# Kernel optimization log

Measured on AMD Instinct MI355X. Metric: run time of the kernel, lower is better.

The kernel has to match this reference:

```python
import jax, jax.numpy as jnp
import numpy as np

N = 50000      # nodes
E = 800000     # edges in adj1/adj2 (avg degree 16)
ED = 400000    # edges after edge-drop
IN = 256       # input feature dim
H = 128        # hidden
H2 = 256       # 2*hidden
GATE = 64


def _xavier(key, shape):
    fan_in, fan_out = shape[0], shape[1]
    lim = np.sqrt(6.0 / (fan_in + fan_out)).astype(np.float32)
    return jax.random.uniform(key, shape, jnp.float32, -lim, lim)


def setup_inputs() -> dict:
    key = jax.random.key(0)
    ks = jax.random.split(key, 20)
    d = {}
    d["x1"] = jax.random.normal(ks[0], (N, IN), jnp.float32)
    d["x2"] = jax.random.normal(ks[1], (N, IN), jnp.float32)
    d["adj1_row"] = jax.random.randint(ks[2], (E,), 0, N, jnp.int32)
    d["adj1_col"] = jax.random.randint(ks[3], (E,), 0, N, jnp.int32)
    d["adj1_val"] = jax.random.uniform(ks[4], (E,), jnp.float32)
    d["adj2_row"] = jax.random.randint(ks[5], (E,), 0, N, jnp.int32)
    d["adj2_col"] = jax.random.randint(ks[6], (E,), 0, N, jnp.int32)
    d["adj2_val"] = jax.random.uniform(ks[7], (E,), jnp.float32)
    d["drop_row"] = jax.random.randint(ks[8], (ED,), 0, N, jnp.int32)
    d["drop_col"] = jax.random.randint(ks[9], (ED,), 0, N, jnp.int32)
    d["drop_val"] = jax.random.uniform(ks[10], (ED,), jnp.float32)
    d["deg"] = jax.random.uniform(ks[11], (N, 1), jnp.float32)
    # GCN layer 0: Linear(IN -> 2H) no bias in fc, plus GCN bias + PReLU
    d["W0"] = _xavier(ks[12], (IN, H2))
    d["b0"] = jnp.zeros((H2,), jnp.float32)
    d["a0"] = jnp.full((1,), 0.25, jnp.float32)  # PReLU param
    # GCN layer 1: Linear(2H -> H)
    d["W1"] = _xavier(ks[13], (H2, H))
    d["b1"] = jnp.zeros((H,), jnp.float32)
    d["a1"] = jnp.full((1,), 0.25, jnp.float32)
    # MLP gate
    d["G1w"] = _xavier(ks[14], (H, GATE))
    d["G1b"] = jnp.zeros((GATE,), jnp.float32)
    d["G2w"] = _xavier(ks[15], (H, GATE))
    d["G2b"] = jnp.zeros((GATE,), jnp.float32)
    d["G3w"] = _xavier(ks[16], (2 * GATE + 1, 1))
    d["G3b"] = jnp.zeros((1,), jnp.float32)
    return d


def _spmm(row, col, val, x, n):
    # sparse adj @ x : gather source features, scale by edge value, scatter-add to rows
    return jax.ops.segment_sum(val[:, None] * x[col], row, num_segments=n)


def _prelu(x, a):
    return jnp.where(x >= 0, x, a * x)


def reference(x1, x2, adj1_row, adj1_col, adj1_val, adj2_row, adj2_col, adj2_val,
              drop_row, drop_col, drop_val, deg,
              W0, b0, a0, W1, b1, a1, G1w, G1b, G2w, G2b, G3w, G3b):
    n = x1.shape[0]

    def gcn(x, row, col, val, W, b, a):
        return _prelu(_spmm(row, col, val, x @ W, n) + b, a)

    def branch(x, row, col, val):
        h = jax.nn.relu(gcn(x, row, col, val, W0, b0, a0))
        return gcn(h, row, col, val, W1, b1, a1)

    # dropout on x1/x2 is identity in eval mode
    h1 = branch(x1, adj1_row, adj1_col, adj1_val)
    h2 = branch(x2, adj1_row, adj1_col, adj1_val)
    h3 = branch(x1, adj2_row, adj2_col, adj2_val)
    h4 = branch(x1, drop_row, drop_col, drop_val)

    # MLP gate on detached h1, h3, deg
    z1 = jax.lax.stop_gradient(h1) @ G1w + G1b
    z2 = jax.lax.stop_gradient(h3) @ G2w + G2b
    w = jnp.concatenate([z1, z2, jax.lax.stop_gradient(deg)], axis=1)
    beta = jax.nn.sigmoid(w @ G3w + G3b)
    return (h1, h2, h3, h4, beta)
```

## Files before the change

kernel.cpp:

```cpp
#include <hip/hip_runtime.h>
#include <hip/hip_bf16.h>

#define H2C 256
#define HDC 128
#define GATEC 64
#define FBSH 9
#define NBF 320
#define EPB 8192
#define EPBH 2048
#define CAPB 10240

typedef unsigned short ushort_t;
typedef unsigned long long ull_t;
typedef __attribute__((ext_vector_type(8))) __bf16 bf16x8;
typedef __attribute__((ext_vector_type(4))) float f32x4;

__device__ inline float bf2f(unsigned short v) {
    union { unsigned u; float f; } t; t.u = ((unsigned)v) << 16; return t.f;
}
__device__ inline unsigned short f2bf(float v) {
    __hip_bfloat16 b = __float2bfloat16(v);
    return *reinterpret_cast<unsigned short*>(&b);
}

__device__ inline void gload_lds16(const void* g, void* l) {
    __builtin_amdgcn_global_load_lds(
        (const __attribute__((address_space(1))) unsigned int*)g,
        (__attribute__((address_space(3))) unsigned int*)l, 16, 0, 0);
}

__global__ __launch_bounds__(256)
void gemm_bf16_mfma(const ushort_t* __restrict__ A, const ushort_t* __restrict__ BT,
                    ushort_t* __restrict__ C, int M, int Nn, int K)
{
    __shared__ ushort_t Alds[128 * 64];
    __shared__ ushort_t Blds[128 * 64];
    const int tid  = threadIdx.x;
    const int w    = tid >> 6;
    const int lane = tid & 63;
    const int wr   = w >> 1;
    const int wc   = w & 1;
    const int bm   = blockIdx.y * 128;
    const int bn   = blockIdx.x * 128;

    f32x4 acc[4][4] = {};

    for (int k0 = 0; k0 < K; k0 += 64) {
        #pragma unroll
        for (int i = 0; i < 4; ++i) {
            const int lin = i * 256 + tid;
            const int r = lin >> 3, p = lin & 7;
            int rm = bm + r; if (rm >= M) rm = M - 1;
            const ushort_t* ga = A + (size_t)rm * K + k0 + ((p ^ (r & 7)) << 3);
            gload_lds16(ga, &Alds[i * 2048 + w * 512]);
        }
        #pragma unroll
        for (int i = 0; i < 4; ++i) {
            const int lin = i * 256 + tid;
            const int r = lin >> 3, p = lin & 7;
            const ushort_t* gb = BT + (size_t)(bn + r) * K + k0 + ((p ^ (r & 7)) << 3);
            gload_lds16(gb, &Blds[i * 2048 + w * 512]);
        }
        __syncthreads();
        #pragma unroll
        for (int kk = 0; kk < 2; ++kk) {
            bf16x8 af[4], bfr[4];
            #pragma unroll
            for (int m = 0; m < 4; ++m) {
                const int r = wr * 64 + m * 16 + (lane & 15);
                const int s = kk * 4 + (lane >> 4);
                af[m] = *reinterpret_cast<const bf16x8*>(&Alds[r * 64 + ((s ^ (r & 7)) << 3)]);
            }
            #pragma unroll
            for (int n = 0; n < 4; ++n) {
                const int r = wc * 64 + n * 16 + (lane & 15);
                const int s = kk * 4 + (lane >> 4);
                bfr[n] = *reinterpret_cast<const bf16x8*>(&Blds[r * 64 + ((s ^ (r & 7)) << 3)]);
            }
            #pragma unroll
            for (int m = 0; m < 4; ++m)
                #pragma unroll
                for (int n = 0; n < 4; ++n)
                    acc[m][n] = __builtin_amdgcn_mfma_f32_16x16x32_bf16(
                        af[m], bfr[n], acc[m][n], 0, 0, 0);
        }
        __syncthreads();
    }

    #pragma unroll
    for (int m = 0; m < 4; ++m) {
        const int row0 = bm + wr * 64 + m * 16 + ((lane >> 4) << 2);
        #pragma unroll
        for (int n = 0; n < 4; ++n) {
            const int col = bn + wc * 64 + n * 16 + (lane & 15);
            #pragma unroll
            for (int q = 0; q < 4; ++q) {
                const int row = row0 + q;
                if (row < M) C[(size_t)row * Nn + col] = f2bf(acc[m][n][q]);
            }
        }
    }
}

__global__ __launch_bounds__(256)
void f2bf_pair_kernel(const float* __restrict__ in1, const float* __restrict__ in2,
                      ushort_t* __restrict__ out, long long n4each)
{
    long long i = (long long)blockIdx.x * blockDim.x + threadIdx.x;
    const long long stride = (long long)gridDim.x * blockDim.x;
    for (; i < 2 * n4each; i += stride) {
        const float* src = (i < n4each) ? in1 : in2;
        const long long k = (i < n4each) ? i : i - n4each;
        const float4 v = reinterpret_cast<const float4*>(src)[k];
        ushort4 o;
        o.x = f2bf(v.x); o.y = f2bf(v.y); o.z = f2bf(v.z); o.w = f2bf(v.w);
        reinterpret_cast<ushort4*>(out)[i] = o;
    }
}

__global__ __launch_bounds__(256)
void transpose_f2bf_kernel(const float* __restrict__ W, ushort_t* __restrict__ WT, int R, int Ccols)
{
    const int i = blockIdx.x * blockDim.x + threadIdx.x;
    if (i >= R * Ccols) return;
    const int c = i / R, r = i % R;
    WT[(size_t)c * R + r] = f2bf(W[(size_t)r * Ccols + c]);
}

__global__ __launch_bounds__(256)
void bucket_hist_kernel(const int* __restrict__ r0, const int* __restrict__ r1_,
                        const int* __restrict__ rD, int E, int ED, int N,
                        int* __restrict__ bcnt)
{
    __shared__ int h[NBF];
    const int tid = threadIdx.x;
    for (int t = tid; t < NBF; t += 256) h[t] = 0;
    __syncthreads();
    const long long tot = 2LL * E + ED;
    const long long base = (long long)blockIdx.x * EPBH;
    #pragma unroll
    for (int k = 0; k < EPBH / 256; ++k) {
        const long long i = base + k * 256 + tid;
        if (i < tot) {
            int vr;
            if (i < E)            vr = r0[i];
            else if (i < 2LL * E) vr = N + r1_[i - E];
            else                  vr = 2 * N + rD[i - 2LL * E];
            atomicAdd(&h[vr >> FBSH], 1);
        }
    }
    __syncthreads();
    for (int t = tid; t < NBF; t += 256)
        if (h[t]) atomicAdd(&bcnt[t], h[t]);
}

__global__ void scan_buckets_kernel(const int* __restrict__ bcnt, int nbu, int tot,
                                    int* __restrict__ boff, int* __restrict__ gcur,
                                    int* __restrict__ g, int NR)
{
    if (threadIdx.x == 0) {
        int acc = 0;
        for (int t = 0; t < nbu; ++t) { boff[t] = acc; gcur[t] = acc; acc += bcnt[t]; }
        boff[nbu] = acc;
        g[NR] = tot;
    }
}

__global__ __launch_bounds__(256)
void bucket_stage_kernel(const int* __restrict__ r0, const int* __restrict__ c0, const float* __restrict__ v0,
                         const int* __restrict__ r1, const int* __restrict__ c1, const float* __restrict__ v1,
                         const int* __restrict__ rD, const int* __restrict__ cD, const float* __restrict__ vD,
                         int E, int ED, int N,
                         int* __restrict__ gcur, ull_t* __restrict__ stg)
{
    __shared__ int hcnt[NBF];
    __shared__ int hbase[NBF];
    const int tid = threadIdx.x;
    for (int t = tid; t < NBF; t += 256) hcnt[t] = 0;
    __syncthreads();
    const long long tot = 2LL * E + ED;
    const long long base = (long long)blockIdx.x * EPB;
    #pragma unroll
    for (int k = 0; k < EPB / 256; ++k) {
        const long long i = base + k * 256 + tid;
        if (i < tot) {
            int vr;
            if (i < E)            vr = r0[i];
            else if (i < 2LL * E) vr = N + r1[i - E];
            else                  vr = 2 * N + rD[i - 2LL * E];
            atomicAdd(&hcnt[vr >> FBSH], 1);
        }
    }
    __syncthreads();
    for (int t = tid; t < NBF; t += 256) {
        const int c = hcnt[t];
        hbase[t] = c ? atomicAdd(&gcur[t], c) : 0;
        hcnt[t] = 0;
    }
    __syncthreads();
    #pragma unroll
    for (int k = 0; k < EPB / 256; ++k) {
        const long long i = base + k * 256 + tid;
        if (i < tot) {
            int vr, cc; float vv;
            if (i < E)            { vr = r0[i];                 cc = c0[i];            vv = v0[i]; }
            else if (i < 2LL * E) { vr = N + r1[i - E];         cc = c1[i - E];        vv = v1[i - E]; }
            else                  { vr = 2 * N + rD[i - 2LL * E]; cc = cD[i - 2LL * E]; vv = vD[i - 2LL * E]; }
            const int fb = vr >> FBSH;
            const int p = hbase[fb] + atomicAdd(&hcnt[fb], 1);
            stg[p] = ((ull_t)(unsigned)vr << 32) | ((unsigned)cc << 16) | f2bf(vv);
        }
    }
}

__global__ __launch_bounds__(256)
void sort_bucket_kernel(const int* __restrict__ boff, int NR,
                        const ull_t* __restrict__ stg,
                        int* __restrict__ g, unsigned* __restrict__ ecv)
{
    __shared__ int hcnt[512];
    __shared__ int hscan[512];
    __shared__ unsigned pay[CAPB];
    const int b = blockIdx.x;
    const int r0 = b << FBSH;
    if (r0 >= NR) return;
    int r1 = r0 + (1 << FBSH); if (r1 > NR) r1 = NR;
    const int nrows = r1 - r0;
    const int base = boff[b], end = boff[b + 1];
    const int bsz = end - base;
    const int tid = threadIdx.x;
    hcnt[tid] = 0; hcnt[tid + 256] = 0;
    __syncthreads();
    for (int i = base + tid; i < end; i += 256)
        atomicAdd(&hcnt[(int)(stg[i] >> 32) - r0], 1);
    __syncthreads();
    hscan[tid] = hcnt[tid]; hscan[tid + 256] = hcnt[tid + 256];
    __syncthreads();
    for (int o = 1; o < 512; o <<= 1) {
        const int a0 = (tid >= o) ? hscan[tid - o] : 0;
        const int a1 = (tid + 256 >= o) ? hscan[tid + 256 - o] : 0;
        __syncthreads();
        hscan[tid] += a0; hscan[tid + 256] += a1;
        __syncthreads();
    }
    if (tid < nrows)       g[r0 + tid]       = base + hscan[tid] - hcnt[tid];
    if (tid + 256 < nrows) g[r0 + tid + 256] = base + hscan[tid + 256] - hcnt[tid + 256];
    hcnt[tid]       = hscan[tid] - hcnt[tid];
    hcnt[tid + 256] = hscan[tid + 256] - hcnt[tid + 256];
    __syncthreads();
    if (bsz <= CAPB) {
        for (int i = base + tid; i < end; i += 256) {
            const ull_t t = stg[i];
            const int p = atomicAdd(&hcnt[(int)(t >> 32) - r0], 1);
            pay[p] = (unsigned)t;
        }
        __syncthreads();
        for (int i = tid; i < bsz; i += 256)
            ecv[base + i] = pay[i];
    } else {
        for (int i = base + tid; i < end; i += 256) {
            const ull_t t = stg[i];
            const int p = atomicAdd(&hcnt[(int)(t >> 32) - r0], 1);
            ecv[base + p] = (unsigned)t;
        }
    }
}

__global__ __launch_bounds__(256)
void spmm_f256(const int* __restrict__ rp, const unsigned* __restrict__ ecv,
               const ushort_t* __restrict__ X, ushort_t* __restrict__ Y,
               const float* __restrict__ bias, const float* __restrict__ ap, int n)
{
    const int r = blockIdx.x * 4 + (threadIdx.x >> 6);
    if (r >= n) return;
    const int lane = threadIdx.x & 63;
    const int half = lane >> 5;
    const int l    = lane & 31;
    const int s = rp[r], e = rp[r + 1];
    float acc[8] = {};
    #pragma unroll 2
    for (int j = s + half; j < e; j += 2) {
        const unsigned ev = ecv[j];
        const float v = bf2f((ushort_t)ev);
        const uint4 x = *reinterpret_cast<const uint4*>(X + (size_t)(ev >> 16) * H2C + l * 8);
        acc[0] += v * bf2f((ushort_t)x.x); acc[1] += v * bf2f((ushort_t)(x.x >> 16));
        acc[2] += v * bf2f((ushort_t)x.y); acc[3] += v * bf2f((ushort_t)(x.y >> 16));
        acc[4] += v * bf2f((ushort_t)x.z); acc[5] += v * bf2f((ushort_t)(x.z >> 16));
        acc[6] += v * bf2f((ushort_t)x.w); acc[7] += v * bf2f((ushort_t)(x.w >> 16));
    }
    #pragma unroll
    for (int k = 0; k < 8; ++k) acc[k] += __shfl_xor(acc[k], 32);
    if (half == 0) {
        const float a = ap[0];
        const int f0 = l * 8;
        const float4 b0v = *reinterpret_cast<const float4*>(bias + f0);
        const float4 b1v = *reinterpret_cast<const float4*>(bias + f0 + 4);
        const float bb[8] = {b0v.x, b0v.y, b0v.z, b0v.w, b1v.x, b1v.y, b1v.z, b1v.w};
        unsigned o[4];
        #pragma unroll
        for (int k = 0; k < 8; k += 2) {
            float tx = acc[k] + bb[k];
            float ty = acc[k + 1] + bb[k + 1];
            tx = tx >= 0.f ? tx : a * tx;  ty = ty >= 0.f ? ty : a * ty;
            tx = fmaxf(tx, 0.f);           ty = fmaxf(ty, 0.f);
            o[k >> 1] = ((unsigned)f2bf(ty) << 16) | f2bf(tx);
        }
        *reinterpret_cast<uint4*>(Y + (size_t)r * H2C + f0) = make_uint4(o[0], o[1], o[2], o[3]);
    }
}

__global__ __launch_bounds__(256)
void spmm_f128(const int* __restrict__ rp, const unsigned* __restrict__ ecv,
               const ushort_t* __restrict__ X, float* __restrict__ Y,
               const float* __restrict__ bias, const float* __restrict__ ap, int n)
{
    const int r = blockIdx.x * 4 + (threadIdx.x >> 6);
    if (r >= n) return;
    const int lane = threadIdx.x & 63;
    const int q = lane >> 4;
    const int l = lane & 15;
    const int s = rp[r], e = rp[r + 1];
    float acc[8] = {};
    #pragma unroll 2
    for (int j = s + q; j < e; j += 4) {
        const unsigned ev = ecv[j];
        const float v = bf2f((ushort_t)ev);
        const uint4 x = *reinterpret_cast<const uint4*>(X + (size_t)(ev >> 16) * HDC + l * 8);
        acc[0] += v * bf2f((ushort_t)x.x); acc[1] += v * bf2f((ushort_t)(x.x >> 16));
        acc[2] += v * bf2f((ushort_t)x.y); acc[3] += v * bf2f((ushort_t)(x.y >> 16));
        acc[4] += v * bf2f((ushort_t)x.z); acc[5] += v * bf2f((ushort_t)(x.z >> 16));
        acc[6] += v * bf2f((ushort_t)x.w); acc[7] += v * bf2f((ushort_t)(x.w >> 16));
    }
    #pragma unroll
    for (int k = 0; k < 8; ++k) {
        acc[k] += __shfl_xor(acc[k], 16);
        acc[k] += __shfl_xor(acc[k], 32);
    }
    if (q == 0) {
        const float a = ap[0];
        const int f0 = l * 8;
        const float4 b0v = *reinterpret_cast<const float4*>(bias + f0);
        const float4 b1v = *reinterpret_cast<const float4*>(bias + f0 + 4);
        const float bb[8] = {b0v.x, b0v.y, b0v.z, b0v.w, b1v.x, b1v.y, b1v.z, b1v.w};
        float o[8];
        #pragma unroll
        for (int k = 0; k < 8; ++k) {
            float t = acc[k] + bb[k];
            o[k] = t >= 0.f ? t : a * t;
        }
        *reinterpret_cast<float4*>(Y + (size_t)r * HDC + f0)     = make_float4(o[0], o[1], o[2], o[3]);
        *reinterpret_cast<float4*>(Y + (size_t)r * HDC + f0 + 4) = make_float4(o[4], o[5], o[6], o[7]);
    }
}

__global__ void gate_pre_kernel(const float* __restrict__ G1w, const float* __restrict__ G1b,
                                const float* __restrict__ G2w, const float* __restrict__ G2b,
                                const float* __restrict__ G3w, const float* __restrict__ G3b,
                                float* __restrict__ U)
{
    const int h = threadIdx.x;
    float s1 = 0.f, s2 = 0.f;
    for (int g = 0; g < GATEC; ++g) {
        s1 += G1w[h * GATEC + g] * G3w[g];
        s2 += G2w[h * GATEC + g] * G3w[GATEC + g];
    }
    U[h] = s1;
    U[HDC + h] = s2;
    if (h == 0) {
        float c = G3b[0];
        for (int g = 0; g < GATEC; ++g)
            c += G1b[g] * G3w[g] + G2b[g] * G3w[GATEC + g];
        U[2 * HDC] = c;
        U[2 * HDC + 1] = G3w[2 * GATEC];
    }
}

__global__ __launch_bounds__(256)
void beta_kernel(const float* __restrict__ h1, const float* __restrict__ h3,
                 const float* __restrict__ deg, const float* __restrict__ U,
                 float* __restrict__ beta, int n)
{
    const int i = blockIdx.x * blockDim.x + threadIdx.x;
    if (i >= n) return;
    const float c = U[2 * HDC], wd = U[2 * HDC + 1];
    float s = c + wd * deg[i];
    const float4* h1p = reinterpret_cast<const float4*>(h1 + (size_t)i * HDC);
    const float4* h3p = reinterpret_cast<const float4*>(h3 + (size_t)i * HDC);
    const float4* u1p = reinterpret_cast<const float4*>(U);
    const float4* u2p = reinterpret_cast<const float4*>(U + HDC);
    #pragma unroll 8
    for (int j = 0; j < HDC / 4; ++j) {
        const float4 a = h1p[j], b = u1p[j];
        s += a.x * b.x + a.y * b.y + a.z * b.z + a.w * b.w;
        const float4 a2 = h3p[j], b2 = u2p[j];
        s += a2.x * b2.x + a2.y * b2.y + a2.z * b2.z + a2.w * b2.w;
    }
    beta[i] = 1.f / (1.f + expf(-s));
}

extern "C" void kernel_launch(void* const* d_in, const int* in_sizes, int n_in,
                              void* d_out, int out_size, void* d_ws, size_t ws_size,
                              hipStream_t stream)
{
    const float* x1  = (const float*)d_in[0];
    const float* x2  = (const float*)d_in[1];
    const int*   a1r = (const int*)d_in[2];
    const int*   a1c = (const int*)d_in[3];
    const float* a1v = (const float*)d_in[4];
    const int*   a2r = (const int*)d_in[5];
    const int*   a2c = (const int*)d_in[6];
    const float* a2v = (const float*)d_in[7];
    const int*   dr  = (const int*)d_in[8];
    const int*   dc  = (const int*)d_in[9];
    const float* dv  = (const float*)d_in[10];
    const float* deg = (const float*)d_in[11];
    const float* W0  = (const float*)d_in[12];
    const float* b0  = (const float*)d_in[13];
    const float* a0  = (const float*)d_in[14];
    const float* W1  = (const float*)d_in[15];
    const float* b1  = (const float*)d_in[16];
    const float* a1p = (const float*)d_in[17];
    const float* G1w = (const float*)d_in[18];
    const float* G1b = (const float*)d_in[19];
    const float* G2w = (const float*)d_in[20];
    const float* G2b = (const float*)d_in[21];
    const float* G3w = (const float*)d_in[22];
    const float* G3b = (const float*)d_in[23];

    const int E  = in_sizes[2];
    const int ED = in_sizes[8];
    const int N  = in_sizes[11];
    const int IN = in_sizes[0] / N;
    const long long TOT = 2LL * E + ED;
    const int NR  = 3 * N;
    const int NBUSED = (NR + (1 << FBSH) - 1) >> FBSH;

    char* base = (char*)d_ws;
    size_t off = 0;
    auto alloc = [&](size_t bytes) -> char* {
        char* p = base + off;
        off += (bytes + 255) & ~(size_t)255;
        return p;
    };
    ushort_t* XW12b = (ushort_t*)alloc((size_t)2 * N * H2C * 2);
    char* R = alloc((size_t)2 * N * H2C * 2);
    ull_t*    stg  = (ull_t*)R;
    ushort_t* Xb12 = (ushort_t*)R;
    ushort_t* Bbb  = (ushort_t*)R;
    ushort_t* Cbb  = (ushort_t*)(R + (size_t)N * H2C * 2);
    ushort_t* W0T  = (ushort_t*)alloc((size_t)H2C * H2C * 2);
    ushort_t* W1T  = (ushort_t*)alloc((size_t)HDC * H2C * 2);
    float*    U    = (float*)alloc(258 * 4);
    int*  g       = (int*)alloc((size_t)(NR + 1) * 4);
    int*  bcnt    = (int*)alloc(NBF * 4);
    int*  boff    = (int*)alloc((NBF + 1) * 4);
    int*  gcur    = (int*)alloc(NBF * 4);
    unsigned* ecv = (unsigned*)alloc((size_t)TOT * 4);

    float* out  = (float*)d_out;
    float* h1   = out;
    float* h2   = out + 1 * (size_t)N * HDC;
    float* h3   = out + 2 * (size_t)N * HDC;
    float* h4   = out + 3 * (size_t)N * HDC;
    float* beta = out + 4 * (size_t)N * HDC;

    gate_pre_kernel<<<1, HDC, 0, stream>>>(G1w, G1b, G2w, G2b, G3w, G3b, U);
    transpose_f2bf_kernel<<<dim3((H2C * H2C + 255) / 256), 256, 0, stream>>>(W0, W0T, H2C, H2C);
    transpose_f2bf_kernel<<<dim3((H2C * HDC + 255) / 256), 256, 0, stream>>>(W1, W1T, H2C, HDC);

    hipMemsetAsync(bcnt, 0, NBF * 4, stream);
    bucket_hist_kernel<<<dim3((unsigned)((TOT + EPBH - 1) / EPBH)), 256, 0, stream>>>(
        a1r, a2r, dr, E, ED, N, bcnt);
    scan_buckets_kernel<<<1, 64, 0, stream>>>(bcnt, NBUSED, (int)TOT, boff, gcur, g, NR);

    bucket_stage_kernel<<<dim3((unsigned)((TOT + EPB - 1) / EPB)), 256, 0, stream>>>(
        a1r, a1c, a1v, a2r, a2c, a2v, dr, dc, dv, E, ED, N, gcur, stg);
    sort_bucket_kernel<<<dim3(NBUSED), 256, 0, stream>>>(boff, NR, stg, g, ecv);

    const int* rp1 = g;
    const int* rp2 = g + N;
    const int* rpD = g + 2 * N;

    f2bf_pair_kernel<<<dim3(2048), 256, 0, stream>>>(x1, x2, Xb12, (long long)N * H2C / 4);
    gemm_bf16_mfma<<<dim3(H2C / 128, (2 * N + 127) / 128), 256, 0, stream>>>(
        Xb12, W0T, XW12b, 2 * N, H2C, IN);

    auto run_branch = [&](const int* rp, const ushort_t* Xsrc, float* hout) {
        spmm_f256<<<dim3((N + 3) / 4), 256, 0, stream>>>(rp, ecv, Xsrc, Bbb, b0, a0, N);
        gemm_bf16_mfma<<<dim3(HDC / 128, (N + 127) / 128), 256, 0, stream>>>(
            Bbb, W1T, Cbb, N, HDC, H2C);
        spmm_f128<<<dim3((N + 3) / 4), 256, 0, stream>>>(rp, ecv, Cbb, hout, b1, a1p, N);
    };

    const ushort_t* XW1b = XW12b;
    const ushort_t* XW2b = XW12b + (size_t)N * H2C;

    run_branch(rp1, XW1b, h1);
    run_branch(rp2, XW1b, h3);
    run_branch(rpD, XW1b, h4);
    run_branch(rp1, XW2b, h2);

    beta_kernel<<<dim3((N + 255) / 256), 256, 0, stream>>>(h1, h3, deg, U, beta, N);
}
```

Measured before the change: 553.2 us.

## Interleave x1/x2 projections per node and fuse shared-adjacency first-layer SpMMs

The first GEMM now writes the x1 and x2 projections into one row-interleaved buffer of 512 features per node. A new dual SpMM kernel walks adj1 once and produces the first-layer activations for both the h1 and h2 branches, with one full wave covering 512 features. The goal is to avoid traversing the same edge list twice and to gather both feature rows with a single contiguous access. The remaining SpMM kernels read the interleaved stride of 512, and their unroll factors go from 2 to 4. The trade-off is a larger workspace and an extra intermediate buffer.

```diff
diff --git a/kernel.cpp b/kernel.cpp
--- a/kernel.cpp
+++ b/kernel.cpp
@@ -29,9 +29,10 @@
         (__attribute__((address_space(3))) unsigned int*)l, 16, 0, 0);
 }
 
+template <bool ILV>
 __global__ __launch_bounds__(256)
 void gemm_bf16_mfma(const ushort_t* __restrict__ A, const ushort_t* __restrict__ BT,
-                    ushort_t* __restrict__ C, int M, int Nn, int K)
+                    ushort_t* __restrict__ C, int M, int Nn, int K, int Mh)
 {
     __shared__ ushort_t Alds[128 * 64];
     __shared__ ushort_t Blds[128 * 64];
@@ -96,7 +97,15 @@
             #pragma unroll
             for (int q = 0; q < 4; ++q) {
                 const int row = row0 + q;
-                if (row < M) C[(size_t)row * Nn + col] = f2bf(acc[m][n][q]);
+                if (row < M) {
+                    if constexpr (ILV) {
+                        const int rr = (row < Mh) ? row : row - Mh;
+                        const int hf = (row < Mh) ? 0 : 1;
+                        C[(size_t)rr * 512 + hf * 256 + col] = f2bf(acc[m][n][q]);
+                    } else {
+                        C[(size_t)row * Nn + col] = f2bf(acc[m][n][q]);
+                    }
+                }
             }
         }
     }
@@ -267,9 +276,48 @@
 }
 
 __global__ __launch_bounds__(256)
-void spmm_f256(const int* __restrict__ rp, const unsigned* __restrict__ ecv,
-               const ushort_t* __restrict__ X, ushort_t* __restrict__ Y,
-               const float* __restrict__ bias, const float* __restrict__ ap, int n)
+void spmm_dual_f256(const int* __restrict__ rp, const unsigned* __restrict__ ecv,
+                    const ushort_t* __restrict__ Xi,
+                    ushort_t* __restrict__ Y1, ushort_t* __restrict__ Y2,
+                    const float* __restrict__ bias, const float* __restrict__ ap, int n)
+{
+    const int r = blockIdx.x * 4 + (threadIdx.x >> 6);
+    if (r >= n) return;
+    const int lane = threadIdx.x & 63;
+    const int s = rp[r], e = rp[r + 1];
+    float acc[8] = {};
+    #pragma unroll 4
+    for (int j = s; j < e; ++j) {
+        const unsigned ev = ecv[j];
+        const float v = bf2f((ushort_t)ev);
+        const uint4 x = *reinterpret_cast<const uint4*>(Xi + (size_t)(ev >> 16) * 512 + lane * 8);
+        acc[0] += v * bf2f((ushort_t)x.x); acc[1] += v * bf2f((ushort_t)(x.x >> 16));
+        acc[2] += v * bf2f((ushort_t)x.y); acc[3] += v * bf2f((ushort_t)(x.y >> 16));
+        acc[4] += v * bf2f((ushort_t)x.z); acc[5] += v * bf2f((ushort_t)(x.z >> 16));
+        acc[6] += v * bf2f((ushort_t)x.w); acc[7] += v * bf2f((ushort_t)(x.w >> 16));
+    }
+    const float a = ap[0];
+    const int f0 = (lane & 31) * 8;
+    ushort_t* Y = (lane < 32) ? Y1 : Y2;
+    const float4 b0v = *reinterpret_cast<const float4*>(bias + f0);
+    const float4 b1v = *reinterpret_cast<const float4*>(bias + f0 + 4);
+    const float bb[8] = {b0v.x, b0v.y, b0v.z, b0v.w, b1v.x, b1v.y, b1v.z, b1v.w};
+    unsigned o[4];
+    #pragma unroll
+    for (int k = 0; k < 8; k += 2) {
+        float tx = acc[k] + bb[k];
+        float ty = acc[k + 1] + bb[k + 1];
+        tx = tx >= 0.f ? tx : a * tx;  ty = ty >= 0.f ? ty : a * ty;
+        tx = fmaxf(tx, 0.f);           ty = fmaxf(ty, 0.f);
+        o[k >> 1] = ((unsigned)f2bf(ty) << 16) | f2bf(tx);
+    }
+    *reinterpret_cast<uint4*>(Y + (size_t)r * H2C + f0) = make_uint4(o[0], o[1], o[2], o[3]);
+}
+
+__global__ __launch_bounds__(256)
+void spmm_f256s(const int* __restrict__ rp, const unsigned* __restrict__ ecv,
+                const ushort_t* __restrict__ Xi, ushort_t* __restrict__ Y,
+                const float* __restrict__ bias, const float* __restrict__ ap, int n)
 {
     const int r = blockIdx.x * 4 + (threadIdx.x >> 6);
     if (r >= n) return;
@@ -278,11 +326,11 @@
     const int l    = lane & 31;
     const int s = rp[r], e = rp[r + 1];
     float acc[8] = {};
-    #pragma unroll 2
+    #pragma unroll 4
     for (int j = s + half; j < e; j += 2) {
         const unsigned ev = ecv[j];
         const float v = bf2f((ushort_t)ev);
-        const uint4 x = *reinterpret_cast<const uint4*>(X + (size_t)(ev >> 16) * H2C + l * 8);
+        const uint4 x = *reinterpret_cast<const uint4*>(Xi + (size_t)(ev >> 16) * 512 + l * 8);
         acc[0] += v * bf2f((ushort_t)x.x); acc[1] += v * bf2f((ushort_t)(x.x >> 16));
         acc[2] += v * bf2f((ushort_t)x.y); acc[3] += v * bf2f((ushort_t)(x.y >> 16));
         acc[4] += v * bf2f((ushort_t)x.z); acc[5] += v * bf2f((ushort_t)(x.z >> 16));
@@ -321,7 +369,7 @@
     const int l = lane & 15;
     const int s = rp[r], e = rp[r + 1];
     float acc[8] = {};
-    #pragma unroll 2
+    #pragma unroll 4
     for (int j = s + q; j < e; j += 4) {
         const unsigned ev = ecv[j];
         const float v = bf2f((ushort_t)ev);
@@ -442,12 +490,13 @@
         off += (bytes + 255) & ~(size_t)255;
         return p;
     };
-    ushort_t* XW12b = (ushort_t*)alloc((size_t)2 * N * H2C * 2);
-    char* R = alloc((size_t)2 * N * H2C * 2);
+    ushort_t* XW12i = (ushort_t*)alloc((size_t)N * 512 * 2);
+    char* R = alloc((size_t)N * 512 * 2 + (size_t)N * HDC * 2);
     ull_t*    stg  = (ull_t*)R;
     ushort_t* Xb12 = (ushort_t*)R;
-    ushort_t* Bbb  = (ushort_t*)R;
+    ushort_t* Bb1  = (ushort_t*)R;
     ushort_t* Cbb  = (ushort_t*)(R + (size_t)N * H2C * 2);
+    ushort_t* Bb2  = (ushort_t*)(R + (size_t)N * H2C * 2 + (size_t)N * HDC * 2);
     ushort_t* W0T  = (ushort_t*)alloc((size_t)H2C * H2C * 2);
     ushort_t* W1T  = (ushort_t*)alloc((size_t)HDC * H2C * 2);
     float*    U    = (float*)alloc(258 * 4);
@@ -482,23 +531,25 @@
     const int* rpD = g + 2 * N;
 
     f2bf_pair_kernel<<<dim3(2048), 256, 0, stream>>>(x1, x2, Xb12, (long long)N * H2C / 4);
-    gemm_bf16_mfma<<<dim3(H2C / 128, (2 * N + 127) / 128), 256, 0, stream>>>(
-        Xb12, W0T, XW12b, 2 * N, H2C, IN);
-
-    auto run_branch = [&](const int* rp, const ushort_t* Xsrc, float* hout) {
-        spmm_f256<<<dim3((N + 3) / 4), 256, 0, stream>>>(rp, ecv, Xsrc, Bbb, b0, a0, N);
-        gemm_bf16_mfma<<<dim3(HDC / 128, (N + 127) / 128), 256, 0, stream>>>(
-            Bbb, W1T, Cbb, N, HDC, H2C);
+    gemm_bf16_mfma<true><<<dim3(H2C / 128, (2 * N + 127) / 128), 256, 0, stream>>>(
+        Xb12, W0T, XW12i, 2 * N, H2C, IN, N);
+
+    spmm_dual_f256<<<dim3((N + 3) / 4), 256, 0, stream>>>(
+        rp1, ecv, XW12i, Bb1, Bb2, b0, a0, N);
+
+    auto run_tail = [&](const int* rp, const ushort_t* Bb, float* hout) {
+        gemm_bf16_mfma<false><<<dim3(HDC / 128, (N + 127) / 128), 256, 0, stream>>>(
+            Bb, W1T, Cbb, N, HDC, H2C, 0);
         spmm_f128<<<dim3((N + 3) / 4), 256, 0, stream>>>(rp, ecv, Cbb, hout, b1, a1p, N);
     };
 
-    const ushort_t* XW1b = XW12b;
-    const ushort_t* XW2b = XW12b + (size_t)N * H2C;
-
-    run_branch(rp1, XW1b, h1);
-    run_branch(rp2, XW1b, h3);
-    run_branch(rpD, XW1b, h4);
-    run_branch(rp1, XW2b, h2);
+    run_tail(rp1, Bb1, h1);
+    run_tail(rp1, Bb2, h2);
+
+    spmm_f256s<<<dim3((N + 3) / 4), 256, 0, stream>>>(rp2, ecv, XW12i, Bb1, b0, a0, N);
+    run_tail(rp2, Bb1, h3);
+    spmm_f256s<<<dim3((N + 3) / 4), 256, 0, stream>>>(rpD, ecv, XW12i, Bb1, b0, a0, N);
+    run_tail(rpD, Bb1, h4);
 
     beta_kernel<<<dim3((N + 255) / 256), 256, 0, stream>>>(h1, h3, deg, U, beta, N);
 }
```

After: 565.8 us. +2.3%, slower.
